# Kernel tuning notes

Measured on AMD Instinct MI355X. Metric: run time of the kernel, lower is better.

The kernel has to match this reference:

```python
import jax, jax.numpy as jnp
import numpy as np

N = 2048
IN_DIM = 256
OUT_DIM = 64
N_HEADS = 8  # head_dim == n_heads required by a: Linear(2*n_heads, 1)
NEG_BIG = -9.0e15


def setup_inputs() -> dict:
    key = jax.random.key(0)
    k1, k2, k3, k4 = jax.random.split(key, 4)
    h = jax.random.normal(k1, (N, IN_DIM), dtype=jnp.float32)
    adj = jax.random.randint(k2, (N, N), 0, 2, dtype=jnp.int32)
    # xavier_uniform with gain=1.414 for W: bound = gain*sqrt(6/(fan_in+fan_out))
    bw = 1.414 * np.sqrt(6.0 / (IN_DIM + OUT_DIM))
    W_w = jax.random.uniform(k3, (OUT_DIM, IN_DIM), minval=-bw, maxval=bw, dtype=jnp.float32)
    W_b = jnp.zeros((OUT_DIM,), dtype=jnp.float32)
    ba = 1.414 * np.sqrt(6.0 / (2 * N_HEADS + 1))
    a_w = jax.random.uniform(k4, (1, 2 * N_HEADS), minval=-ba, maxval=ba, dtype=jnp.float32)
    a_b = jnp.zeros((1,), dtype=jnp.float32)
    return {"h": h, "adj": adj, "W_w": W_w, "W_b": W_b, "a_w": a_w, "a_b": a_b}


def reference(h, adj, W_w, W_b, a_w, a_b):
    H = a_w.shape[1] // 2
    out_dim = W_w.shape[0]
    Dh = out_dim // H  # == H by construction
    n = h.shape[0]
    wh = h @ W_w.T + W_b                      # [N, out_dim]
    wh_head = wh.reshape(n, H, Dh)            # [N, H, Dh]
    aL = a_w[0, :Dh]                           # applies to source node i features
    aR = a_w[0, Dh:]                           # applies to node j features
    e_i = jnp.einsum('nhd,d->nh', wh_head, aL)  # [N, H]
    e_j = jnp.einsum('nhd,d->nh', wh_head, aR)  # [N, H]
    # scores[i,j,h] without materializing the N*N concat tensor
    scores = e_i[:, None, :] + e_j[None, :, :] + a_b[0]   # [N, N, H]
    scores = jnp.where(scores >= 0, scores, 0.2 * scores)  # leaky_relu(0.2)
    masked = jnp.where(adj[:, :, None] > 0, scores, NEG_BIG)
    att = jax.nn.softmax(masked, axis=1)       # normalize over j
    # out[h,i,d] = sum_j att[i,j,h] * wh_head[j,h,d]
    out = jnp.einsum('ijh,jhd->hid', att, wh_head)  # [H, N, Dh]
    out = jax.nn.elu(out)
    return out.reshape(-1, out_dim)            # faithful to .view(-1, out_dim)
```

## Files before the change

### kernel.cpp

```cpp
#include <hip/hip_runtime.h>
#include <math.h>

#define NN 2048
#define INDIM 256
#define ODIM 64
#define NH 8
#define DHD 8
#define LOG2E 1.44269504088896340736f
#define IBLK 4

__global__ __launch_bounds__(256) void gat_pre(
    const float* __restrict__ h, const float* __restrict__ Ww,
    const float* __restrict__ Wb, const float* __restrict__ aw,
    const float* __restrict__ ab,
    unsigned short* __restrict__ whb, float* __restrict__ eiL,
    float* __restrict__ ejL)
{
    __shared__ float sH[IBLK][INDIM];
    const int t = threadIdx.x;
    const int n0 = blockIdx.x * 4;
    ((float4*)&sH[0][0])[t] = ((const float4*)(h + (size_t)n0 * INDIM))[t];
    __syncthreads();

    const int o  = t & 63;
    const int wv = t >> 6;
    const int n  = n0 + wv;
    const float4* w4 = (const float4*)(Ww + (size_t)o * INDIM);
    float acc = 0.f;
#pragma unroll 8
    for (int k = 0; k < INDIM / 4; ++k) {
        const float4 wk = w4[k];
        const float4 hv = *(const float4*)&sH[wv][k * 4];
        acc = fmaf(wk.x, hv.x, acc); acc = fmaf(wk.y, hv.y, acc);
        acc = fmaf(wk.z, hv.z, acc); acc = fmaf(wk.w, hv.w, acc);
    }
    acc += Wb[o];

    {
        unsigned int u = __float_as_uint(acc);
        unsigned int r = (u + 0x7FFF + ((u >> 16) & 1)) >> 16;
        whb[(size_t)n * ODIM + o] = (unsigned short)r;
    }

    const int d = o & 7;
    float pi = acc * aw[d];
    float pj = acc * aw[NH + d];
    pi += __shfl_xor(pi, 1, 64); pj += __shfl_xor(pj, 1, 64);
    pi += __shfl_xor(pi, 2, 64); pj += __shfl_xor(pj, 2, 64);
    pi += __shfl_xor(pi, 4, 64); pj += __shfl_xor(pj, 4, 64);
    if (d == 0) {
        const int hd = o >> 3;
        eiL[n * NH + hd] = (pi + ab[0]) * LOG2E;
        ejL[n * NH + hd] = pj * LOG2E;
    }
}

__global__ __launch_bounds__(512) void gat_main(
    const int* __restrict__ adj, const unsigned short* __restrict__ whb,
    const float* __restrict__ eiL, const float* __restrict__ ejL,
    float* __restrict__ out)
{
    __shared__ unsigned char s_bits[NN];
    __shared__ float s_red[8][8][IBLK][9];
    const int t  = threadIdx.x;
    const int i0 = blockIdx.x * IBLK;

    {
        unsigned int b0 = 0, b1 = 0, b2 = 0, b3 = 0;
#pragma unroll
        for (int i = 0; i < IBLK; ++i) {
            const int4 v = *(const int4*)(adj + (size_t)(i0 + i) * NN + 4 * t);
            b0 |= (v.x != 0) << i;
            b1 |= (v.y != 0) << i;
            b2 |= (v.z != 0) << i;
            b3 |= (v.w != 0) << i;
        }
        ((uchar4*)s_bits)[t] = make_uchar4((unsigned char)b0, (unsigned char)b1,
                                           (unsigned char)b2, (unsigned char)b3);
    }
    __syncthreads();

    const int hh = t & 7;
    const int jj = t >> 3;
    float eih[IBLK];
#pragma unroll
    for (int i = 0; i < IBLK; ++i) eih[i] = eiL[(i0 + i) * NH + hh];

    float den[IBLK] = {0.f, 0.f, 0.f, 0.f};
    float acc[IBLK][DHD];
#pragma unroll
    for (int i = 0; i < IBLK; ++i)
#pragma unroll
        for (int d = 0; d < DHD; ++d) acc[i][d] = 0.f;

    const float* ejp = ejL + jj * NH + hh;
    const uint4* wp  = (const uint4*)whb + jj * NH + hh;
    const unsigned char* bp = s_bits + jj;

    float pe = *ejp;
    uint4 pw = *wp;

#pragma unroll 2
    for (int it = 0; it < NN / 64; ++it) {
        const float ce = pe;
        const uint4 cw = pw;
        const int bits = *bp;
        ejp += 64 * NH; wp += 64 * NH; bp += 64;
        pe = *ejp;
        pw = *wp;

        float e[IBLK];
#pragma unroll
        for (int i = 0; i < IBLK; ++i) {
            float s = eih[i] + ce;
            s = fmaxf(s, 0.2f * s);
            s = (bits & (1 << i)) ? s : -192.0f;
            e[i] = __builtin_amdgcn_exp2f(s);
            den[i] += e[i];
        }
#pragma unroll
        for (int q = 0; q < 4; ++q) {
            const unsigned int w = (&cw.x)[q];
            const float lo = __uint_as_float(w << 16);
            const float hi = __uint_as_float(w & 0xFFFF0000u);
#pragma unroll
            for (int i = 0; i < IBLK; ++i) {
                acc[i][2 * q]     = fmaf(e[i], lo, acc[i][2 * q]);
                acc[i][2 * q + 1] = fmaf(e[i], hi, acc[i][2 * q + 1]);
            }
        }
    }

#pragma unroll
    for (int m = 8; m <= 32; m <<= 1) {
#pragma unroll
        for (int i = 0; i < IBLK; ++i) {
            den[i] += __shfl_xor(den[i], m, 64);
#pragma unroll
            for (int d = 0; d < DHD; ++d)
                acc[i][d] += __shfl_xor(acc[i][d], m, 64);
        }
    }
    const int lane = t & 63;
    const int wv   = t >> 6;
    if (lane < 8) {
#pragma unroll
        for (int i = 0; i < IBLK; ++i) {
#pragma unroll
            for (int d = 0; d < DHD; ++d) s_red[wv][lane][i][d] = acc[i][d];
            s_red[wv][lane][i][8] = den[i];
        }
    }
    __syncthreads();

    if (t < 256) {
        const int i  = t >> 6;
        const int hD = (t >> 3) & 7;
        const int d  = t & 7;
        float v = 0.f, dn = 0.f;
#pragma unroll
        for (int w2 = 0; w2 < 8; ++w2) {
            v  += s_red[w2][hD][i][d];
            dn += s_red[w2][hD][i][8];
        }
        float r = v / dn;
        r = (r > 0.f) ? r : expm1f(r);
        out[(size_t)hD * (NN * DHD) + (size_t)(i0 + i) * DHD + d] = r;
    }
}

extern "C" void kernel_launch(void* const* d_in, const int* in_sizes, int n_in,
                              void* d_out, int out_size, void* d_ws, size_t ws_size,
                              hipStream_t stream) {
    const float* h   = (const float*)d_in[0];
    const int*   adj = (const int*)d_in[1];
    const float* Ww  = (const float*)d_in[2];
    const float* Wb  = (const float*)d_in[3];
    const float* aw  = (const float*)d_in[4];
    const float* ab  = (const float*)d_in[5];
    float* out = (float*)d_out;

    char* ws = (char*)d_ws;
    unsigned short* whb = (unsigned short*)ws;
    float* eiL  = (float*)(ws + 262144);
    float* ejL  = (float*)(ws + 327680);

    gat_pre<<<NN / 4, 256, 0, stream>>>(h, Ww, Wb, aw, ab, whb, eiL, ejL);
    gat_main<<<NN / IBLK, 512, 0, stream>>>(adj, whb, eiL, ejL, out);
}
```

Measured before the change: 43.14 us.

## Compute attention aggregation with bf16 MFMA and split-J partial reduction

Replaces the scalar FMA attention-weighted aggregation with 16x16x32 bf16 MFMA instructions, packing exp weights into bf16 A fragments. A constant ones column in the B operand computes the softmax denominator in the same instruction. The node features and scores are transposed so MFMA operands load contiguously. The j dimension is split into four quarters across blocks, with a new finalize kernel that reduces the partials and applies the ELU. This adds a third launch and a partial-sum buffer in global memory, and rounds the attention weights to bf16.

After: 41.31 us, median of 2. 1.04x faster.

```diff
diff --git a/kernel.cpp b/kernel.cpp
--- a/kernel.cpp
+++ b/kernel.cpp
@@ -7,16 +7,21 @@
 #define NH 8
 #define DHD 8
 #define LOG2E 1.44269504088896340736f
-#define IBLK 4
+#define JQ 4
+#define JQL (NN / JQ)
+#define ITILE 16
+
+typedef __attribute__((ext_vector_type(4))) float f32x4;
+typedef __attribute__((ext_vector_type(8))) short s16x8;
 
 __global__ __launch_bounds__(256) void gat_pre(
     const float* __restrict__ h, const float* __restrict__ Ww,
     const float* __restrict__ Wb, const float* __restrict__ aw,
     const float* __restrict__ ab,
-    unsigned short* __restrict__ whb, float* __restrict__ eiL,
-    float* __restrict__ ejL)
+    unsigned short* __restrict__ whT, float* __restrict__ eiT,
+    float* __restrict__ ejT)
 {
-    __shared__ float sH[IBLK][INDIM];
+    __shared__ float sH[4][INDIM];
     const int t = threadIdx.x;
     const int n0 = blockIdx.x * 4;
     ((float4*)&sH[0][0])[t] = ((const float4*)(h + (size_t)n0 * INDIM))[t];
@@ -39,7 +44,7 @@
     {
         unsigned int u = __float_as_uint(acc);
         unsigned int r = (u + 0x7FFF + ((u >> 16) & 1)) >> 16;
-        whb[(size_t)n * ODIM + o] = (unsigned short)r;
+        whT[(size_t)o * NN + n] = (unsigned short)r;
     }
 
     const int d = o & 7;
@@ -50,123 +55,112 @@
     pi += __shfl_xor(pi, 4, 64); pj += __shfl_xor(pj, 4, 64);
     if (d == 0) {
         const int hd = o >> 3;
-        eiL[n * NH + hd] = (pi + ab[0]) * LOG2E;
-        ejL[n * NH + hd] = pj * LOG2E;
+        eiT[(size_t)hd * NN + n] = (pi + ab[0]) * LOG2E;
+        ejT[(size_t)hd * NN + n] = pj * LOG2E;
     }
 }
 
-__global__ __launch_bounds__(512) void gat_main(
-    const int* __restrict__ adj, const unsigned short* __restrict__ whb,
-    const float* __restrict__ eiL, const float* __restrict__ ejL,
-    float* __restrict__ out)
+__global__ __launch_bounds__(512) void gat_mfma(
+    const int* __restrict__ adj, const unsigned short* __restrict__ whT,
+    const float* __restrict__ eiT, const float* __restrict__ ejT,
+    float* __restrict__ pacc)
 {
-    __shared__ unsigned char s_bits[NN];
-    __shared__ float s_red[8][8][IBLK][9];
+    __shared__ unsigned int s_mask[ITILE][17];
+    __shared__ float s_ej[NH][JQL];
     const int t  = threadIdx.x;
-    const int i0 = blockIdx.x * IBLK;
+    const int it = blockIdx.x >> 2;
+    const int jq = blockIdx.x & 3;
+    const int i0 = it * ITILE;
+    const int j0 = jq * JQL;
 
-    {
-        unsigned int b0 = 0, b1 = 0, b2 = 0, b3 = 0;
+    if (t < ITILE * 16) {
+        const int row = t >> 4, w = t & 15;
+        const int* ap = adj + (size_t)(i0 + row) * NN + j0 + w * 32;
+        unsigned int b = 0;
 #pragma unroll
-        for (int i = 0; i < IBLK; ++i) {
-            const int4 v = *(const int4*)(adj + (size_t)(i0 + i) * NN + 4 * t);
-            b0 |= (v.x != 0) << i;
-            b1 |= (v.y != 0) << i;
-            b2 |= (v.z != 0) << i;
-            b3 |= (v.w != 0) << i;
+        for (int q = 0; q < 8; ++q) {
+            const int4 v = ((const int4*)ap)[q];
+            b |= (unsigned)(v.x != 0) << (q * 4 + 0);
+            b |= (unsigned)(v.y != 0) << (q * 4 + 1);
+            b |= (unsigned)(v.z != 0) << (q * 4 + 2);
+            b |= (unsigned)(v.w != 0) << (q * 4 + 3);
         }
-        ((uchar4*)s_bits)[t] = make_uchar4((unsigned char)b0, (unsigned char)b1,
-                                           (unsigned char)b2, (unsigned char)b3);
+        s_mask[row][w] = b;
+    }
+    for (int idx = t; idx < NH * JQL; idx += 512) {
+        const int hh = idx >> 9, jl = idx & 511;
+        s_ej[hh][jl] = ejT[(size_t)hh * NN + j0 + jl];
     }
     __syncthreads();
 
-    const int hh = t & 7;
-    const int jj = t >> 3;
-    float eih[IBLK];
+    const int l   = t & 63;
+    const int hh  = t >> 6;
+    const int row = l & 15;
+    const int g   = l >> 4;
+    const float eirow = eiT[(size_t)hh * NN + i0 + row];
+
+    const unsigned short* vbase = whT + ((size_t)(hh * DHD + row)) * NN + j0 + g * 8;
+    union { unsigned int u[4]; s16x8 v; } bconst;
+    {
+        const unsigned int cv = (row == 8) ? 0x3F803F80u : 0u;
+        bconst.u[0] = cv; bconst.u[1] = cv; bconst.u[2] = cv; bconst.u[3] = cv;
+    }
+
+    f32x4 acc = {0.f, 0.f, 0.f, 0.f};
+
+    for (int step = 0; step < JQL / 32; ++step) {
+        const unsigned int mbyte = (s_mask[row][step] >> (g * 8)) & 0xFFu;
+        const float4 ea = *(const float4*)&s_ej[hh][step * 32 + g * 8];
+        const float4 eb = *(const float4*)&s_ej[hh][step * 32 + g * 8 + 4];
+
+        float p[8];
+        p[0] = eirow + ea.x; p[1] = eirow + ea.y;
+        p[2] = eirow + ea.z; p[3] = eirow + ea.w;
+        p[4] = eirow + eb.x; p[5] = eirow + eb.y;
+        p[6] = eirow + eb.z; p[7] = eirow + eb.w;
 #pragma unroll
-    for (int i = 0; i < IBLK; ++i) eih[i] = eiL[(i0 + i) * NH + hh];
+        for (int i = 0; i < 8; ++i) {
+            float s = fmaxf(p[i], 0.2f * p[i]);
+            s = (mbyte & (1u << i)) ? s : -192.0f;
+            p[i] = __builtin_amdgcn_exp2f(s);
+        }
+        union { unsigned int u[4]; s16x8 v; } af;
+#pragma unroll
+        for (int q = 0; q < 4; ++q)
+            asm("v_cvt_pk_bf16_f32 %0, %1, %2"
+                : "=v"(af.u[q]) : "v"(p[2 * q]), "v"(p[2 * q + 1]));
 
-    float den[IBLK] = {0.f, 0.f, 0.f, 0.f};
-    float acc[IBLK][DHD];
-#pragma unroll
-    for (int i = 0; i < IBLK; ++i)
-#pragma unroll
-        for (int d = 0; d < DHD; ++d) acc[i][d] = 0.f;
+        s16x8 bf;
+        if (row < DHD) bf = *(const s16x8*)(vbase + step * 32);
+        else           bf = bconst.v;
 
-    const float* ejp = ejL + jj * NH + hh;
-    const uint4* wp  = (const uint4*)whb + jj * NH + hh;
-    const unsigned char* bp = s_bits + jj;
-
-    float pe = *ejp;
-    uint4 pw = *wp;
-
-#pragma unroll 2
-    for (int it = 0; it < NN / 64; ++it) {
-        const float ce = pe;
-        const uint4 cw = pw;
-        const int bits = *bp;
-        ejp += 64 * NH; wp += 64 * NH; bp += 64;
-        pe = *ejp;
-        pw = *wp;
-
-        float e[IBLK];
-#pragma unroll
-        for (int i = 0; i < IBLK; ++i) {
-            float s = eih[i] + ce;
-            s = fmaxf(s, 0.2f * s);
-            s = (bits & (1 << i)) ? s : -192.0f;
-            e[i] = __builtin_amdgcn_exp2f(s);
-            den[i] += e[i];
-        }
-#pragma unroll
-        for (int q = 0; q < 4; ++q) {
-            const unsigned int w = (&cw.x)[q];
-            const float lo = __uint_as_float(w << 16);
-            const float hi = __uint_as_float(w & 0xFFFF0000u);
-#pragma unroll
-            for (int i = 0; i < IBLK; ++i) {
-                acc[i][2 * q]     = fmaf(e[i], lo, acc[i][2 * q]);
-                acc[i][2 * q + 1] = fmaf(e[i], hi, acc[i][2 * q + 1]);
-            }
-        }
+        acc = __builtin_amdgcn_mfma_f32_16x16x32_bf16(af.v, bf, acc, 0, 0, 0);
     }
 
 #pragma unroll
-    for (int m = 8; m <= 32; m <<= 1) {
+    for (int r = 0; r < 4; ++r) {
+        const int orow = g * 4 + r;
+        pacc[(((size_t)(jq * NH + hh)) * NN + (i0 + orow)) * 16 + row] = acc[r];
+    }
+}
+
+__global__ __launch_bounds__(256) void gat_fin(
+    const float* __restrict__ pacc, float* __restrict__ out)
+{
+    const int gid = blockIdx.x * 256 + threadIdx.x;
+    const int d  = gid & 7;
+    const int i  = (gid >> 3) & (NN - 1);
+    const int hh = gid >> 14;
+    float v = 0.f, dn = 0.f;
 #pragma unroll
-        for (int i = 0; i < IBLK; ++i) {
-            den[i] += __shfl_xor(den[i], m, 64);
-#pragma unroll
-            for (int d = 0; d < DHD; ++d)
-                acc[i][d] += __shfl_xor(acc[i][d], m, 64);
-        }
+    for (int jq = 0; jq < JQ; ++jq) {
+        const float* p = pacc + (((size_t)(jq * NH + hh)) * NN + i) * 16;
+        v  += p[d];
+        dn += p[8];
     }
-    const int lane = t & 63;
-    const int wv   = t >> 6;
-    if (lane < 8) {
-#pragma unroll
-        for (int i = 0; i < IBLK; ++i) {
-#pragma unroll
-            for (int d = 0; d < DHD; ++d) s_red[wv][lane][i][d] = acc[i][d];
-            s_red[wv][lane][i][8] = den[i];
-        }
-    }
-    __syncthreads();
-
-    if (t < 256) {
-        const int i  = t >> 6;
-        const int hD = (t >> 3) & 7;
-        const int d  = t & 7;
-        float v = 0.f, dn = 0.f;
-#pragma unroll
-        for (int w2 = 0; w2 < 8; ++w2) {
-            v  += s_red[w2][hD][i][d];
-            dn += s_red[w2][hD][i][8];
-        }
-        float r = v / dn;
-        r = (r > 0.f) ? r : expm1f(r);
-        out[(size_t)hD * (NN * DHD) + (size_t)(i0 + i) * DHD + d] = r;
-    }
+    float r = v / dn;
+    r = (r > 0.f) ? r : expm1f(r);
+    out[gid] = r;
 }
 
 extern "C" void kernel_launch(void* const* d_in, const int* in_sizes, int n_in,
@@ -181,10 +175,12 @@
     float* out = (float*)d_out;
 
     char* ws = (char*)d_ws;
-    unsigned short* whb = (unsigned short*)ws;
-    float* eiL  = (float*)(ws + 262144);
-    float* ejL  = (float*)(ws + 327680);
+    unsigned short* whT = (unsigned short*)ws;
+    float* eiT  = (float*)(ws + 262144);
+    float* ejT  = (float*)(ws + 327680);
+    float* pacc = (float*)(ws + 393216);
 
-    gat_pre<<<NN / 4, 256, 0, stream>>>(h, Ww, Wb, aw, ab, whb, eiL, ejL);
-    gat_main<<<NN / IBLK, 512, 0, stream>>>(adj, whb, eiL, ejL, out);
+    gat_pre<<<NN / 4, 256, 0, stream>>>(h, Ww, Wb, aw, ab, whT, eiT, ejT);
+    gat_mfma<<<(NN / ITILE) * JQ, 512, 0, stream>>>(adj, whT, eiT, ejT, pacc);
+    gat_fin<<<NN * ODIM / 256, 256, 0, stream>>>(pacc, out);
 }
```
